# Kernel optimization log

Measured on AMD Instinct MI355X. Metric: run time of the kernel, lower is better.

Reference implementation:

```python
import jax, jax.numpy as jnp
import numpy as np

D_MODEL, STATE, N_EXP, VOCAB = 1024, 16, 4, 32000
B, L = 4, 2048
EPS = 1e-5


def setup_inputs() -> dict:
    key = jax.random.key(0)
    ks = jax.random.split(key, 20)
    d, s, e, f = D_MODEL, STATE, N_EXP, 4 * D_MODEL
    sc = 0.02
    inp = {
        "x": jax.random.normal(ks[0], (B, L, d), jnp.float32),
        "A_log": jnp.log(jax.random.uniform(ks[1], (d, s)) * 0.9 + 0.1),
        "D_param": jnp.ones((d,), jnp.float32),
        "Wd": jax.random.normal(ks[2], (d, d)) * sc,
        "bd": jnp.zeros((d,)),
        "WB": jax.random.normal(ks[3], (d, s)) * sc,
        "bB": jnp.zeros((s,)),
        "WC": jax.random.normal(ks[4], (d, s)) * sc,
        "bC": jnp.zeros((s,)),
        "Wr": jax.random.normal(ks[5], (d, e)) * sc,
        "br": jnp.zeros((e,)),
        "up_w": jax.random.normal(ks[6], (e, d, f)) * sc,
        "up_b": jnp.zeros((e, f)),
        "down_w": jax.random.normal(ks[7], (e, f, d)) * sc,
        "down_b": jnp.zeros((e, d)),
        "ln_w": jnp.ones((d,)),
        "ln_b": jnp.zeros((d,)),
    }
    return inp


def reference(x, A_log, D_param, Wd, bd, WB, bB, WC, bC, Wr, br,
              up_w, up_b, down_w, down_b, ln_w, ln_b):
    Bb, Ll, d = x.shape
    delta = jax.nn.softplus(jnp.einsum('bld,de->ble', x, Wd) + bd)   # [B,L,D]
    Bm = jnp.einsum('bld,ds->bls', x, WB) + bB                        # [B,L,S]
    Cm = jnp.einsum('bld,ds->bls', x, WC) + bC                        # [B,L,S]
    A = -jnp.exp(A_log)                                               # [D,S]

    def step(h, inps):
        x_t, d_t, B_t, C_t = inps                                     # [B,D],[B,D],[B,S],[B,S]
        bar_A = jnp.exp(jnp.minimum(d_t[:, :, None] * A, 2.0))        # [B,D,S]
        bar_B = jnp.clip(d_t[:, :, None] * B_t[:, None, :], -2.0, 2.0)
        h = jnp.clip(bar_A * h + bar_B * x_t[:, :, None], -100.0, 100.0)
        y = jnp.sum(h * C_t[:, None, :], axis=-1) + x_t * D_param     # [B,D]
        return h, y

    h0 = jnp.zeros((Bb, d, STATE), x.dtype)
    xs = (jnp.swapaxes(x, 0, 1), jnp.swapaxes(delta, 0, 1),
          jnp.swapaxes(Bm, 0, 1), jnp.swapaxes(Cm, 0, 1))
    _, ys = jax.lax.scan(step, h0, xs)                                # ys: [L,B,D]
    ssm_out = jnp.swapaxes(ys, 0, 1)                                  # [B,L,D]

    flat = ssm_out.reshape(-1, d)                                     # [N,D]
    routing = jax.nn.softmax(flat @ Wr + br, axis=1)                  # [N,E]
    top1_w = jnp.max(routing, axis=1)                                 # [N]
    top1_i = jnp.argmax(routing, axis=1)                              # [N]

    hid = jax.nn.silu(jnp.einsum('nd,edf->enf', flat, up_w) + up_b[:, None, :])
    all_out = jnp.einsum('enf,efd->end', hid, down_w) + down_b[:, None, :]  # [E,N,D]
    sel = jnp.take_along_axis(jnp.swapaxes(all_out, 0, 1),
                              top1_i[:, None, None], axis=1)[:, 0, :]  # [N,D]
    moe_out = (sel * top1_w[:, None]).reshape(Bb, Ll, d)

    out = ssm_out + moe_out
    mu = jnp.mean(out, axis=-1, keepdims=True)
    var = jnp.mean((out - mu) ** 2, axis=-1, keepdims=True)
    return (out - mu) * jax.lax.rsqrt(var + EPS) * ln_w + ln_b
```

## Files before the change

kernel.cpp:

```cpp
#include <hip/hip_runtime.h>

typedef __attribute__((ext_vector_type(4))) float f32x4;
typedef __attribute__((ext_vector_type(8))) short short8;
typedef __attribute__((ext_vector_type(8))) unsigned short ushort8;
typedef __attribute__((ext_vector_type(4))) unsigned short ushort4v;

#define DEV __device__ __forceinline__

constexpr int NTOK = 8192;
constexpr int NCP  = 1152;
constexpr int MAXTILES = 68;
constexpr int NPAD = MAXTILES * 128;
constexpr int NCHUNK = 16;
constexpr int CLEN = 2048 / NCHUNK;

DEV unsigned short f2bf(float f) {
  unsigned int u = __builtin_bit_cast(unsigned int, f);
  u += 0x7FFFu + ((u >> 16) & 1u);
  return (unsigned short)(u >> 16);
}
DEV float bf2f(unsigned short h) {
  unsigned int u = ((unsigned int)h) << 16;
  return __builtin_bit_cast(float, u);
}

DEV void gload16(const unsigned short* g, unsigned short* l) {
  __builtin_amdgcn_global_load_lds(
      (const __attribute__((address_space(1))) unsigned int*)g,
      (__attribute__((address_space(3))) unsigned int*)l, 16, 0, 0);
}

__global__ __launch_bounds__(256) void conv_x_k(const float* __restrict__ x,
    unsigned short* __restrict__ xh, unsigned short* __restrict__ xl) {
  int i = (blockIdx.x * 256 + threadIdx.x) * 4;
  f32x4 v = *(const f32x4*)(x + i);
  ushort4v hv, lv;
#pragma unroll
  for (int j = 0; j < 4; ++j) {
    unsigned short hh = f2bf(v[j]);
    hv[j] = hh;
    lv[j] = f2bf(v[j] - bf2f(hh));
  }
  *(ushort4v*)(xh + i) = hv;
  *(ushort4v*)(xl + i) = lv;
}

__global__ __launch_bounds__(256) void conv_w_k(const float* __restrict__ Wd,
    const float* __restrict__ WB, const float* __restrict__ WC,
    unsigned short* __restrict__ wh, unsigned short* __restrict__ wl) {
  int o = blockIdx.x * 256 + threadIdx.x;
  int k = o & 1023, n = o >> 10;
  float v = 0.f;
  if (n < 1024) v = Wd[k * 1024 + n];
  else if (n < 1040) v = WB[k * 16 + (n - 1024)];
  else if (n < 1056) v = WC[k * 16 + (n - 1040)];
  unsigned short hh = f2bf(v);
  wh[o] = hh;
  wl[o] = f2bf(v - bf2f(hh));
}

__global__ __launch_bounds__(256) void trans_k(const float* __restrict__ in,
    unsigned short* __restrict__ out, int R, int C) {
  __shared__ float tile[32][33];
  int e = blockIdx.z;
  int r0 = blockIdx.y * 32, c0 = blockIdx.x * 32;
  int r = threadIdx.x >> 5, cc = threadIdx.x & 31;
  const float* src = in + ((size_t)e * R + r0) * C + c0;
#pragma unroll
  for (int j = 0; j < 4; ++j) tile[r + j * 8][cc] = src[(size_t)(r + j * 8) * C + cc];
  __syncthreads();
  unsigned short* dst = out + ((size_t)e * C + c0) * R + r0;
#pragma unroll
  for (int j = 0; j < 4; ++j) dst[(size_t)(r + j * 8) * R + cc] = f2bf(tile[cc][r + j * 8]);
}

template<int MODE>
__global__ __launch_bounds__(256) void gemm_k(
    const unsigned short* __restrict__ A, const unsigned short* __restrict__ A2,
    const unsigned short* __restrict__ Bm, const unsigned short* __restrict__ B2,
    float* __restrict__ outF, unsigned short* __restrict__ outH,
    const float* __restrict__ bias, const float* __restrict__ b1, const float* __restrict__ b2,
    const int* __restrict__ perm, const float* __restrict__ t1w,
    const int* __restrict__ tile_e, const int* __restrict__ tile_r0,
    const int* __restrict__ tile_ve, const int* __restrict__ n_tiles)
{
  constexpr int K = (MODE == 2) ? 4096 : 1024;
  constexpr int KT = K / 64;
  constexpr bool SPLIT = (MODE == 0);
  __shared__ __align__(16) unsigned short lA[(SPLIT ? 2 : 1) * 128 * 64];
  __shared__ __align__(16) unsigned short lB[(SPLIT ? 2 : 1) * 128 * 64];

  const int t = threadIdx.x;
  const int bx = blockIdx.x;
  const int by = blockIdx.y;
  int e = 0, row0 = 0, vend = 0;
  if constexpr (MODE == 0) {
    row0 = by * 128;
  } else {
    if (by >= *n_tiles) return;
    e = tile_e[by]; row0 = tile_r0[by]; vend = tile_ve[by];
  }
  (void)vend;

  const int w = t >> 6, lane = t & 63;
  const int srow = w * 32 + (lane >> 3);
  const int scol = (lane & 7) * 8;
  const unsigned short* ap[4];
  const unsigned short* bp[4];
  ptrdiff_t da = 0, db = 0;
  if constexpr (SPLIT) { da = A2 - A; db = B2 - Bm; }
#pragma unroll
  for (int c = 0; c < 4; ++c) {
    int r = row0 + srow + c * 8;
    if constexpr (MODE == 1) {
      int tok = perm[r];
      ap[c] = A + (size_t)tok * 1024 + scol;
    } else if constexpr (MODE == 2) {
      ap[c] = A + (size_t)r * 4096 + scol;
    } else {
      ap[c] = A + (size_t)r * 1024 + scol;
    }
    int cb = bx * 128 + srow + c * 8;
    if constexpr (MODE == 0) bp[c] = Bm + (size_t)cb * 1024 + scol;
    else if constexpr (MODE == 1) bp[c] = Bm + ((size_t)e * 4096 + cb) * 1024 + scol;
    else bp[c] = Bm + ((size_t)e * 1024 + cb) * 4096 + scol;
  }

  const int wm = w >> 1, wn = w & 1;
  const int lr = lane & 15, lk = (lane >> 4) * 8;
  int aoffe[4], boffe[4];
#pragma unroll
  for (int i = 0; i < 4; ++i) {
    aoffe[i] = (wm * 64 + i * 16 + lr) * 64 + lk;
    boffe[i] = (wn * 64 + i * 16 + lr) * 64 + lk;
  }

  f32x4 acc[4][4];
#pragma unroll
  for (int i = 0; i < 4; ++i)
#pragma unroll
    for (int j = 0; j < 4; ++j) acc[i][j] = (f32x4)(0.f);

  for (int kt = 0; kt < KT; ++kt) {
    __syncthreads();
#pragma unroll
    for (int c = 0; c < 4; ++c) {
      unsigned short* ldst = lA + w * 2048 + c * 512;
      unsigned short* ldst2 = lB + w * 2048 + c * 512;
      gload16(ap[c], ldst);
      gload16(bp[c], ldst2);
      if constexpr (SPLIT) {
        gload16(ap[c] + da, ldst + 8192);
        gload16(bp[c] + db, ldst2 + 8192);
      }
      ap[c] += 64; bp[c] += 64;
    }
    __syncthreads();
#pragma unroll
    for (int kk = 0; kk < 2; ++kk) {
      short8 af[4], bfv[4], afl[4], bfl[4];
#pragma unroll
      for (int i = 0; i < 4; ++i) {
        af[i]  = *(const short8*)(lA + aoffe[i] + kk * 32);
        bfv[i] = *(const short8*)(lB + boffe[i] + kk * 32);
        if constexpr (SPLIT) {
          afl[i] = *(const short8*)(lA + 8192 + aoffe[i] + kk * 32);
          bfl[i] = *(const short8*)(lB + 8192 + boffe[i] + kk * 32);
        }
      }
#pragma unroll
      for (int mi = 0; mi < 4; ++mi)
#pragma unroll
        for (int ni = 0; ni < 4; ++ni) {
          acc[mi][ni] = __builtin_amdgcn_mfma_f32_16x16x32_bf16(af[mi], bfv[ni], acc[mi][ni], 0, 0, 0);
          if constexpr (SPLIT) {
            acc[mi][ni] = __builtin_amdgcn_mfma_f32_16x16x32_bf16(afl[mi], bfv[ni], acc[mi][ni], 0, 0, 0);
            acc[mi][ni] = __builtin_amdgcn_mfma_f32_16x16x32_bf16(af[mi], bfl[ni], acc[mi][ni], 0, 0, 0);
          }
        }
    }
  }

#pragma unroll
  for (int mi = 0; mi < 4; ++mi) {
#pragma unroll
    for (int ni = 0; ni < 4; ++ni) {
      int col = bx * 128 + wn * 64 + ni * 16 + lr;
#pragma unroll
      for (int q = 0; q < 4; ++q) {
        int rl = wm * 64 + mi * 16 + (lane >> 4) * 4 + q;
        float v = acc[mi][ni][q];
        if constexpr (MODE == 0) {
          if (col < 1056) {
            float v2;
            if (col < 1024) {
              float z = v + bias[col];
              v2 = fmaxf(z, 0.f) + __logf(1.f + __expf(-fabsf(z)));
            } else if (col < 1040) {
              v2 = v + b1[col - 1024];
            } else {
              v2 = v + b2[col - 1040];
            }
            outF[(size_t)(row0 + rl) * NCP + col] = v2;
          }
        } else if constexpr (MODE == 1) {
          float z = v + bias[e * 4096 + col];
          float sg = 1.f / (1.f + __expf(-z));
          outH[(size_t)(row0 + rl) * 4096 + col] = f2bf(z * sg);
        } else {
          int pos = row0 + rl;
          if (pos < vend) {
            int tok = perm[pos];
            float val = (v + bias[e * 1024 + col]) * t1w[tok];
            outF[(size_t)tok * 1024 + col] = val;
          }
        }
      }
    }
  }
}

constexpr int SPF = 4;

template<int PASS>
__global__ __launch_bounds__(256) void scan_p(
    const float* __restrict__ P, const float* __restrict__ x,
    const float* __restrict__ A_log, const float* __restrict__ D_param,
    float* __restrict__ Ap, float* __restrict__ He, const float* __restrict__ Hi,
    float* __restrict__ ssm, unsigned short* __restrict__ ssmbf)
{
  const int t = threadIdx.x;
  const int s = t & 15, dlane = t >> 4;
  const int blk = blockIdx.x;
  const int c  = blk & 15;
  const int dg = (blk >> 4) & 63;
  const int b  = blk >> 10;
  const int d  = dg * 16 + dlane;
  const float Ads = -__expf(A_log[d * 16 + s]);
  const float Dp = D_param[d];
  const float* Pb = P + ((size_t)b * 2048 + (size_t)c * CLEN) * NCP;
  const float* xb = x + ((size_t)b * 2048 + (size_t)c * CLEN) * 1024;
  const size_t sidx = (size_t)c * 65536 + ((size_t)b * 1024 + d) * 16 + s;

  float h = (PASS == 1) ? 0.f : Hi[sidx];
  float ap = 1.f;

  float dl0[SPF], br0[SPF], cr0[SPF], xr0[SPF];
  auto LOADB = [&](int base, float* dd, float* bb, float* cc2, float* xx) {
#pragma unroll
    for (int j = 0; j < SPF; ++j) {
      const float* Pt = Pb + (size_t)(base + j) * NCP;
      dd[j] = Pt[d];
      bb[j] = Pt[1024 + s];
      if constexpr (PASS == 3) cc2[j] = Pt[1040 + s];
      xx[j] = xb[(size_t)(base + j) * 1024 + d];
    }
  };
  LOADB(0, dl0, br0, cr0, xr0);
  size_t obase = ((size_t)b * 2048 + (size_t)c * CLEN) * 1024 + d;
  constexpr int NBAT = CLEN / SPF;
  for (int bb = 0; bb < NBAT; ++bb) {
    float dl1[SPF], br1[SPF], cr1[SPF], xr1[SPF];
    if (bb + 1 < NBAT) LOADB((bb + 1) * SPF, dl1, br1, cr1, xr1);
#pragma unroll
    for (int j = 0; j < SPF; ++j) {
      float delta = dl0[j];
      float barA = __expf(delta * Ads);
      float barB = fminf(fmaxf(delta * br0[j], -2.f), 2.f);
      h = fminf(fmaxf(barA * h + barB * xr0[j], -100.f), 100.f);
      if constexpr (PASS == 1) {
        ap *= barA;
      } else {
        float y = h * cr0[j];
        y += __shfl_xor(y, 1); y += __shfl_xor(y, 2);
        y += __shfl_xor(y, 4); y += __shfl_xor(y, 8);
        if (s == 0) {
          float val = y + xr0[j] * Dp;
          size_t o = obase + (size_t)(bb * SPF + j) * 1024;
          ssm[o] = val;
          ssmbf[o] = f2bf(val);
        }
      }
    }
    if (bb + 1 < NBAT) {
#pragma unroll
      for (int j = 0; j < SPF; ++j) { dl0[j]=dl1[j]; br0[j]=br1[j]; cr0[j]=cr1[j]; xr0[j]=xr1[j]; }
    }
  }
  if constexpr (PASS == 1) {
    Ap[sidx] = ap;
    He[sidx] = h;
  }
}

__global__ __launch_bounds__(256) void scan_c(const float* __restrict__ Ap,
    const float* __restrict__ He, float* __restrict__ Hi)
{
  int i = blockIdx.x * 256 + threadIdx.x;
  float h = 0.f;
#pragma unroll
  for (int c = 0; c < NCHUNK; ++c) {
    size_t idx = (size_t)c * 65536 + i;
    Hi[idx] = h;
    h = Ap[idx] * h + He[idx];
  }
}

__global__ __launch_bounds__(256) void route_k(
    const float* __restrict__ ssm, const float* __restrict__ Wr, const float* __restrict__ br,
    float* __restrict__ t1w, int* __restrict__ t1i, int* __restrict__ counts)
{
  int w = threadIdx.x >> 6, lane = threadIdx.x & 63;
  int n = blockIdx.x * 4 + w;
  const float* row = ssm + (size_t)n * 1024;
  float a0 = 0, a1 = 0, a2 = 0, a3 = 0;
  for (int i = lane; i < 1024; i += 64) {
    float v = row[i];
    f32x4 wr = *(const f32x4*)(Wr + i * 4);
    a0 += v * wr[0]; a1 += v * wr[1]; a2 += v * wr[2]; a3 += v * wr[3];
  }
#pragma unroll
  for (int off = 32; off; off >>= 1) {
    a0 += __shfl_xor(a0, off); a1 += __shfl_xor(a1, off);
    a2 += __shfl_xor(a2, off); a3 += __shfl_xor(a3, off);
  }
  a0 += br[0]; a1 += br[1]; a2 += br[2]; a3 += br[3];
  float m = a0; int idx = 0;
  if (a1 > m) { m = a1; idx = 1; }
  if (a2 > m) { m = a2; idx = 2; }
  if (a3 > m) { m = a3; idx = 3; }
  float denom = __expf(a0 - m) + __expf(a1 - m) + __expf(a2 - m) + __expf(a3 - m);
  if (lane == 0) {
    t1w[n] = 1.f / denom;
    t1i[n] = idx;
    atomicAdd(&counts[idx], 1);
  }
}

__global__ void build_k(int* misc, int* perm)
{
  if (threadIdx.x != 0 || blockIdx.x != 0) return;
  int* counts = misc; int* cursors = misc + 4; int* base = misc + 8;
  int* ntiles = misc + 12; int* te = misc + 16; int* tr = misc + 96; int* tv = misc + 176;
  int bpos = 0, tt = 0;
  for (int e = 0; e < 4; ++e) {
    base[e] = bpos; cursors[e] = 0;
    int c = counts[e];
    int nt = (c + 127) >> 7;
    for (int i = 0; i < nt; ++i) { te[tt] = e; tr[tt] = bpos + i * 128; tv[tt] = bpos + c; ++tt; }
    for (int p = bpos + c; p < bpos + nt * 128; ++p) perm[p] = 0;
    bpos += nt * 128;
  }
  *ntiles = tt;
}

__global__ __launch_bounds__(256) void scatter_k(const int* __restrict__ t1i,
    int* misc, int* __restrict__ perm)
{
  int n = blockIdx.x * 256 + threadIdx.x;
  int e = t1i[n];
  int pos = atomicAdd(&misc[4 + e], 1);
  perm[misc[8 + e] + pos] = n;
}

__global__ __launch_bounds__(256) void ln_k(
    float* __restrict__ out, const float* __restrict__ ssm,
    const float* __restrict__ lnw, const float* __restrict__ lnb)
{
  __shared__ float red[8];
  int n = blockIdx.x, t = threadIdx.x;
  size_t base = (size_t)n * 1024 + t * 4;
  f32x4 a = *(const f32x4*)(out + base);
  f32x4 bsm = *(const f32x4*)(ssm + base);
  float o[4]; float sum = 0, sq = 0;
#pragma unroll
  for (int j = 0; j < 4; ++j) { o[j] = a[j] + bsm[j]; sum += o[j]; sq += o[j] * o[j]; }
#pragma unroll
  for (int off = 32; off; off >>= 1) { sum += __shfl_xor(sum, off); sq += __shfl_xor(sq, off); }
  int w = t >> 6;
  if ((t & 63) == 0) { red[w] = sum; red[4 + w] = sq; }
  __syncthreads();
  sum = red[0] + red[1] + red[2] + red[3];
  sq  = red[4] + red[5] + red[6] + red[7];
  float mu = sum * (1.f / 1024.f);
  float var = sq * (1.f / 1024.f) - mu * mu;
  float rs = rsqrtf(var + 1e-5f);
  f32x4 r;
#pragma unroll
  for (int j = 0; j < 4; ++j) {
    int c = t * 4 + j;
    r[j] = (o[j] - mu) * rs * lnw[c] + lnb[c];
  }
  *(f32x4*)(out + base) = r;
}

extern "C" void kernel_launch(void* const* d_in, const int* in_sizes, int n_in,
                              void* d_out, int out_size, void* d_ws, size_t ws_size,
                              hipStream_t stream)
{
  (void)in_sizes; (void)n_in; (void)out_size;
  const float* x       = (const float*)d_in[0];
  const float* A_log   = (const float*)d_in[1];
  const float* D_param = (const float*)d_in[2];
  const float* Wd      = (const float*)d_in[3];
  const float* bd      = (const float*)d_in[4];
  const float* WB      = (const float*)d_in[5];
  const float* bB      = (const float*)d_in[6];
  const float* WC      = (const float*)d_in[7];
  const float* bC      = (const float*)d_in[8];
  const float* Wr      = (const float*)d_in[9];
  const float* br      = (const float*)d_in[10];
  const float* up_w    = (const float*)d_in[11];
  const float* up_b    = (const float*)d_in[12];
  const float* down_w  = (const float*)d_in[13];
  const float* down_b  = (const float*)d_in[14];
  const float* ln_w    = (const float*)d_in[15];
  const float* ln_b    = (const float*)d_in[16];
  float* out = (float*)d_out;

  char* ws = (char*)d_ws;
  size_t off = 0;
  auto alloc = [&](size_t bytes) { size_t o = off; off += (bytes + 255) & ~(size_t)255; return o; };
  size_t oXh  = alloc((size_t)NTOK * 1024 * 2);
  size_t oXl  = alloc((size_t)NTOK * 1024 * 2);
  size_t oWh  = alloc((size_t)NCP * 1024 * 2);
  size_t oWl  = alloc((size_t)NCP * 1024 * 2);
  size_t oP   = alloc((size_t)NTOK * NCP * 4);
  size_t oSSM = alloc((size_t)NTOK * 1024 * 4);
  size_t oSBF = alloc((size_t)NTOK * 1024 * 2);
  size_t oUp  = alloc((size_t)4 * 4096 * 1024 * 2);
  size_t oDn  = alloc((size_t)4 * 4096 * 1024 * 2);
  size_t oHid = alloc((size_t)NPAD * 4096 * 2);
  size_t oT1w = alloc((size_t)NTOK * 4);
  size_t oT1i = alloc((size_t)NTOK * 4);
  size_t oPerm= alloc((size_t)NPAD * 4);
  size_t oMisc= alloc(1024);
  if (ws_size < off) return;

  unsigned short* Xh  = (unsigned short*)(ws + oXh);
  unsigned short* Xl  = (unsigned short*)(ws + oXl);
  unsigned short* Wh  = (unsigned short*)(ws + oWh);
  unsigned short* Wl  = (unsigned short*)(ws + oWl);
  float*          Pf  = (float*)(ws + oP);
  float*          SSM = (float*)(ws + oSSM);
  unsigned short* SBF = (unsigned short*)(ws + oSBF);
  unsigned short* UpT = (unsigned short*)(ws + oUp);
  unsigned short* DnT = (unsigned short*)(ws + oDn);
  unsigned short* Hid = (unsigned short*)(ws + oHid);
  float*          T1w = (float*)(ws + oT1w);
  int*            T1i = (int*)(ws + oT1i);
  int*            perm= (int*)(ws + oPerm);
  int*            misc= (int*)(ws + oMisc);
  float*          ApB = (float*)(ws + oHid);
  float*          HeB = ApB + (size_t)NCHUNK * 65536;
  float*          HiB = HeB + (size_t)NCHUNK * 65536;

  hipMemsetAsync(misc, 0, 16, stream);
  conv_x_k <<<8192, 256, 0, stream>>>(x, Xh, Xl);
  conv_w_k <<<4608, 256, 0, stream>>>(Wd, WB, WC, Wh, Wl);
  trans_k<<<dim3(128, 32, 4), 256, 0, stream>>>(up_w, UpT, 1024, 4096);
  trans_k<<<dim3(32, 128, 4), 256, 0, stream>>>(down_w, DnT, 4096, 1024);

  gemm_k<0><<<dim3(9, 64), 256, 0, stream>>>(Xh, Xl, Wh, Wl, Pf, nullptr,
      bd, bB, bC, nullptr, nullptr, nullptr, nullptr, nullptr, nullptr);

  scan_p<1><<<4096, 256, 0, stream>>>(Pf, x, A_log, D_param, ApB, HeB, nullptr, nullptr, nullptr);
  scan_c   <<<256, 256, 0, stream>>>(ApB, HeB, HiB);
  scan_p<3><<<4096, 256, 0, stream>>>(Pf, x, A_log, D_param, nullptr, nullptr, HiB, SSM, SBF);

  route_k<<<2048, 256, 0, stream>>>(SSM, Wr, br, T1w, T1i, misc);
  build_k<<<1, 1, 0, stream>>>(misc, perm);
  scatter_k<<<32, 256, 0, stream>>>(T1i, misc, perm);

  gemm_k<1><<<dim3(32, MAXTILES), 256, 0, stream>>>(SBF, nullptr, UpT, nullptr,
      nullptr, Hid, up_b, nullptr, nullptr, perm, nullptr, misc + 16, misc + 96, misc + 176, misc + 12);
  gemm_k<2><<<dim3(8, MAXTILES), 256, 0, stream>>>(Hid, nullptr, DnT, nullptr,
      out, nullptr, down_b, nullptr, nullptr, perm, T1w, misc + 16, misc + 96, misc + 176, misc + 12);

  ln_k<<<8192, 256, 0, stream>>>(out, SSM, ln_w, ln_b);
}
```

Measured before the change: 899.7 us.

## Double-buffer LDS tiles in GEMM kernel to overlap global loads with MFMA

Adds a two-stage LDS ping-pong in the GEMM kernel: the next K-slice is issued with direct global-to-LDS loads while MFMAs run on the current buffer, and one barrier per iteration replaces two. For the split-precision mode the K tile shrinks to 32 so that doubled buffers still fit in LDS. The cost is more LDS per block, which may lower occupancy, and smaller K steps in mode 0.

```diff
diff --git a/kernel.cpp b/kernel.cpp
--- a/kernel.cpp
+++ b/kernel.cpp
@@ -85,10 +85,16 @@
     const int* __restrict__ tile_ve, const int* __restrict__ n_tiles)
 {
   constexpr int K = (MODE == 2) ? 4096 : 1024;
-  constexpr int KT = K / 64;
   constexpr bool SPLIT = (MODE == 0);
-  __shared__ __align__(16) unsigned short lA[(SPLIT ? 2 : 1) * 128 * 64];
-  __shared__ __align__(16) unsigned short lB[(SPLIT ? 2 : 1) * 128 * 64];
+  constexpr int BK   = SPLIT ? 32 : 64;
+  constexpr int KT   = K / BK;
+  constexpr int TILE = 128 * BK;
+  constexpr int BUFE = TILE * (SPLIT ? 2 : 1);
+  constexpr int LPR  = BK / 8;
+  constexpr int RPC  = 64 / LPR;
+  constexpr int NCH  = 32 / RPC;
+  __shared__ __align__(16) unsigned short lA[2 * BUFE];
+  __shared__ __align__(16) unsigned short lB[2 * BUFE];
 
   const int t = threadIdx.x;
   const int bx = blockIdx.x;
@@ -103,15 +109,15 @@
   (void)vend;
 
   const int w = t >> 6, lane = t & 63;
-  const int srow = w * 32 + (lane >> 3);
-  const int scol = (lane & 7) * 8;
-  const unsigned short* ap[4];
-  const unsigned short* bp[4];
+  const int srow = w * 32 + lane / LPR;
+  const int scol = (lane % LPR) * 8;
+  const unsigned short* ap[NCH];
+  const unsigned short* bp[NCH];
   ptrdiff_t da = 0, db = 0;
   if constexpr (SPLIT) { da = A2 - A; db = B2 - Bm; }
 #pragma unroll
-  for (int c = 0; c < 4; ++c) {
-    int r = row0 + srow + c * 8;
+  for (int c = 0; c < NCH; ++c) {
+    int r = row0 + srow + c * RPC;
     if constexpr (MODE == 1) {
       int tok = perm[r];
       ap[c] = A + (size_t)tok * 1024 + scol;
@@ -120,7 +126,7 @@
     } else {
       ap[c] = A + (size_t)r * 1024 + scol;
     }
-    int cb = bx * 128 + srow + c * 8;
+    int cb = bx * 128 + srow + c * RPC;
     if constexpr (MODE == 0) bp[c] = Bm + (size_t)cb * 1024 + scol;
     else if constexpr (MODE == 1) bp[c] = Bm + ((size_t)e * 4096 + cb) * 1024 + scol;
     else bp[c] = Bm + ((size_t)e * 1024 + cb) * 4096 + scol;
@@ -131,8 +137,8 @@
   int aoffe[4], boffe[4];
 #pragma unroll
   for (int i = 0; i < 4; ++i) {
-    aoffe[i] = (wm * 64 + i * 16 + lr) * 64 + lk;
-    boffe[i] = (wn * 64 + i * 16 + lr) * 64 + lk;
+    aoffe[i] = (wm * 64 + i * 16 + lr) * BK + lk;
+    boffe[i] = (wn * 64 + i * 16 + lr) * BK + lk;
   }
 
   f32x4 acc[4][4];
@@ -141,31 +147,37 @@
 #pragma unroll
     for (int j = 0; j < 4; ++j) acc[i][j] = (f32x4)(0.f);
 
+  auto STAGE = [&](int buf, int kt) {
+    unsigned short* la = lA + buf * BUFE + w * (32 * BK);
+    unsigned short* lb = lB + buf * BUFE + w * (32 * BK);
+#pragma unroll
+    for (int c = 0; c < NCH; ++c) {
+      gload16(ap[c] + kt * BK, la + c * 512);
+      gload16(bp[c] + kt * BK, lb + c * 512);
+      if constexpr (SPLIT) {
+        gload16(ap[c] + da + kt * BK, la + TILE + c * 512);
+        gload16(bp[c] + db + kt * BK, lb + TILE + c * 512);
+      }
+    }
+  };
+
+  STAGE(0, 0);
+  __syncthreads();
+  int cur = 0;
   for (int kt = 0; kt < KT; ++kt) {
-    __syncthreads();
-#pragma unroll
-    for (int c = 0; c < 4; ++c) {
-      unsigned short* ldst = lA + w * 2048 + c * 512;
-      unsigned short* ldst2 = lB + w * 2048 + c * 512;
-      gload16(ap[c], ldst);
-      gload16(bp[c], ldst2);
-      if constexpr (SPLIT) {
-        gload16(ap[c] + da, ldst + 8192);
-        gload16(bp[c] + db, ldst2 + 8192);
-      }
-      ap[c] += 64; bp[c] += 64;
-    }
-    __syncthreads();
-#pragma unroll
-    for (int kk = 0; kk < 2; ++kk) {
+    if (kt + 1 < KT) STAGE(cur ^ 1, kt + 1);
+    const unsigned short* cA = lA + cur * BUFE;
+    const unsigned short* cB = lB + cur * BUFE;
+#pragma unroll
+    for (int kk = 0; kk < BK / 32; ++kk) {
       short8 af[4], bfv[4], afl[4], bfl[4];
 #pragma unroll
       for (int i = 0; i < 4; ++i) {
-        af[i]  = *(const short8*)(lA + aoffe[i] + kk * 32);
-        bfv[i] = *(const short8*)(lB + boffe[i] + kk * 32);
+        af[i]  = *(const short8*)(cA + aoffe[i] + kk * 32);
+        bfv[i] = *(const short8*)(cB + boffe[i] + kk * 32);
         if constexpr (SPLIT) {
-          afl[i] = *(const short8*)(lA + 8192 + aoffe[i] + kk * 32);
-          bfl[i] = *(const short8*)(lB + 8192 + boffe[i] + kk * 32);
+          afl[i] = *(const short8*)(cA + TILE + aoffe[i] + kk * 32);
+          bfl[i] = *(const short8*)(cB + TILE + boffe[i] + kk * 32);
         }
       }
 #pragma unroll
@@ -179,6 +191,8 @@
           }
         }
     }
+    __syncthreads();
+    cur ^= 1;
   }
 
 #pragma unroll
```

New measurement: 995.1 us. 1.11x slower.
